# Performance work log

Hardware: AMD Instinct MI355X
Metric: run time of the kernel (lower is better)

## Reference

```python
import jax, jax.numpy as jnp
import numpy as np

N, X_DIM, Z_DIM, H = 4096, 256, 128, 512
NUM_ACTIONS = 4
TEMPERATURE = 0.1


def _init_linear(key, fan_in, fan_out):
    kw, kb = jax.random.split(key)
    bound = 1.0 / np.sqrt(fan_in)
    W = jax.random.uniform(kw, (fan_in, fan_out), minval=-bound, maxval=bound, dtype=jnp.float32)
    b = jax.random.uniform(kb, (fan_out,), minval=-bound, maxval=bound, dtype=jnp.float32)
    return W, b


def setup_inputs() -> dict:
    key = jax.random.key(0)
    ks = jax.random.split(key, 9)
    s = jax.random.normal(ks[0], (N, X_DIM), dtype=jnp.float32)
    sp = jax.random.normal(ks[1], (N, X_DIM), dtype=jnp.float32)
    a = jax.random.randint(ks[2], (N,), 0, NUM_ACTIONS)
    a1h = jax.nn.one_hot(a, NUM_ACTIONS, dtype=jnp.float32)
    # phi: x_dim -> 512 -> 512 -> z_dim
    pW0, pb0 = _init_linear(ks[3], X_DIM, H)
    pW1, pb1 = _init_linear(ks[4], H, H)
    pW2, pb2 = _init_linear(ks[5], H, Z_DIM)
    # g: x_dim + 4 -> 512 -> 512 -> z_dim
    gW0, gb0 = _init_linear(ks[6], X_DIM + NUM_ACTIONS, H)
    gW1, gb1 = _init_linear(ks[7], H, H)
    gW2, gb2 = _init_linear(ks[8], H, Z_DIM)
    return {"s": s, "sp": sp, "a1h": a1h,
            "pW0": pW0, "pb0": pb0, "pW1": pW1, "pb1": pb1, "pW2": pW2, "pb2": pb2,
            "gW0": gW0, "gb0": gb0, "gW1": gW1, "gb1": gb1, "gW2": gW2, "gb2": gb2}


def _mlp(x, W0, b0, W1, b1, W2, b2):
    h = jax.nn.relu(x @ W0 + b0)
    h = jax.nn.relu(h @ W1 + b1)
    return h @ W2 + b2


def reference(s, sp, a1h, pW0, pb0, pW1, pb1, pW2, pb2, gW0, gb0, gW1, gb1, gW2, gb2):
    z = _mlp(s, pW0, pb0, pW1, pb1, pW2, pb2)                      # [N, D]
    zpos = _mlp(jnp.concatenate([sp, a1h], axis=-1), gW0, gb0, gW1, gb1, gW2, gb2)  # [N, D]
    # -||z_i - zpos_j||^2 / T via the GEMM trick (avoids the [N,N,D] diff tensor)
    sq_z = jnp.sum(z * z, axis=-1, keepdims=True)                  # [N, 1]
    sq_p = jnp.sum(zpos * zpos, axis=-1)                            # [N]
    logits = -(sq_z + sq_p[None, :] - 2.0 * z @ zpos.T) / TEMPERATURE  # [N, N]
    # cross-entropy with targets = arange(N): diagonal is the positive
    log_probs = jax.nn.log_softmax(logits, axis=-1)
    loss = -jnp.mean(jnp.diagonal(log_probs))
    return loss
```

## Files before the change

kernel.cpp:

```cpp
#include <hip/hip_runtime.h>
#include <math.h>

#define NR 4096
#define ZD 128
#define HD 512
#define NJR 32
#define INV_T 10.0f

typedef __attribute__((ext_vector_type(8))) short bf16x8;
typedef __attribute__((ext_vector_type(4))) short short4v;
typedef __attribute__((ext_vector_type(4))) float f32x4;

typedef const unsigned int __attribute__((address_space(1)))* gas_t;
typedef unsigned int __attribute__((address_space(3)))* las_t;

__device__ __forceinline__ unsigned short f2bf(float f) {
  union { float f; unsigned u; } v; v.f = f;
  unsigned r = v.u + 0x7fff + ((v.u >> 16) & 1);
  return (unsigned short)(r >> 16);
}
__device__ __forceinline__ float bf2f(unsigned short b) {
  union { unsigned u; float f; } v; v.u = ((unsigned)b) << 16;
  return v.f;
}


__global__ __launch_bounds__(256) void prep(
    const float* __restrict__ s, const float* __restrict__ sp,
    const float* __restrict__ a1h,
    unsigned short* __restrict__ Sb, unsigned short* __restrict__ SPb,
    int* __restrict__ aidx,
    const float* __restrict__ pW0, unsigned short* __restrict__ pW0t,
    const float* __restrict__ pW1, unsigned short* __restrict__ pW1t,
    const float* __restrict__ pW2, unsigned short* __restrict__ pW2t,
    const float* __restrict__ gW0, unsigned short* __restrict__ gW0t,
    const float* __restrict__ gW1, unsigned short* __restrict__ gW1t,
    const float* __restrict__ gW2, unsigned short* __restrict__ gW2t,
    float* __restrict__ out) {
  int b = blockIdx.x, tid = threadIdx.x;
  if (b < 16) {
    int r = b * 256 + tid;
    int a = 0;
#pragma unroll
    for (int j = 0; j < 4; ++j) if (a1h[(size_t)r * 4 + j] > 0.5f) a = j;
    aidx[r] = a;
    if (b == 0 && tid == 0) out[0] = 0.f;
    return;
  }
  const int idx8 = tid & 127;
  const int h = idx8 & 1, p = idx8 >> 1, hi = p >> 4, l15 = p & 15;
  if (b < 2064) {
    const float* src = (b < 1040) ? s : sp;
    unsigned short* dst = (b < 1040) ? Sb : SPb;
    int lb = (b < 1040) ? b - 16 : b - 1040;
    int s0 = lb * 2 + (tid >> 7);
    int rf = s0 >> 3, ks = s0 & 7;
    int row = rf * 16 + l15, c0 = ks * 32 + hi * 4 + h * 16;
    float4 v = *(const float4*)&src[(size_t)row * 256 + c0];
    short4v o = { (short)f2bf(v.x), (short)f2bf(v.y), (short)f2bf(v.z), (short)f2bf(v.w) };
    *(short4v*)((char*)dst + (size_t)s0 * 1024 + idx8 * 8) = o;
    return;
  }
  int local = b - 2064;
  const float* W; unsigned short* Wt; int N, ksh;
  if (local < 128)      { W = pW0; Wt = pW0t; N = 512; ksh = 3; }
  else if (local < 384) { W = pW1; Wt = pW1t; N = 512; ksh = 4; local -= 128; }
  else if (local < 448) { W = pW2; Wt = pW2t; N = 128; ksh = 4; local -= 384; }
  else if (local < 576) { W = gW0; Wt = gW0t; N = 512; ksh = 3; local -= 448; }
  else if (local < 832) { W = gW1; Wt = gW1t; N = 512; ksh = 4; local -= 576; }
  else                  { W = gW2; Wt = gW2t; N = 128; ksh = 4; local -= 832; }
  int s0 = local * 2 + (tid >> 7);
  int rf = s0 >> ksh, ks = s0 & ((1 << ksh) - 1);
  int n = rf * 16 + l15, k0 = ks * 32 + hi * 4 + h * 16;
  short4v o = { (short)f2bf(W[(size_t)(k0 + 0) * N + n]),
                (short)f2bf(W[(size_t)(k0 + 1) * N + n]),
                (short)f2bf(W[(size_t)(k0 + 2) * N + n]),
                (short)f2bf(W[(size_t)(k0 + 3) * N + n]) };
  *(short4v*)((char*)Wt + (size_t)s0 * 1024 + idx8 * 8) = o;
}

template <bool RELU, bool GB, bool SQ, int K>
__global__ __launch_bounds__(256) void gemm_lds(
    const unsigned short* __restrict__ A0, const unsigned short* __restrict__ A1,
    const unsigned short* __restrict__ W0, const unsigned short* __restrict__ W1,
    const float* __restrict__ b0, const float* __restrict__ b1,
    unsigned short* __restrict__ C0, unsigned short* __restrict__ C1,
    float* __restrict__ sqp2, int N,
    const int* __restrict__ aidx, const float* __restrict__ gW0f) {
  __shared__ char As[2][16384];
  __shared__ char Bs[2][16384];
  constexpr int KS = K >> 5;
  constexpr int NSTEP = K >> 6;
  const int tid = threadIdx.x, lane = tid & 63, w = tid >> 6;
  const int wm = w >> 1, wn = w & 1;
  const int z = blockIdx.z;
  const char* Ab = (const char*)(z ? A1 : A0);
  const char* Wb = (const char*)(z ? W1 : W0);
  const float* bias = z ? b1 : b0;
  char* Cb = (char*)(z ? C1 : C0);
  const int bm = blockIdx.x * 128, bn = blockIdx.y * 128;
  const int lane16 = lane * 16;

  const char* asrc[4];
  const char* bsrc[4];
#pragma unroll
  for (int u = 0; u < 4; ++u) {
    const int sl = w * 4 + u;
    asrc[u] = Ab + (size_t)(((bm >> 4) + (sl >> 1)) * KS + (sl & 1)) * 1024 + lane16;
    bsrc[u] = Wb + (size_t)(((bn >> 4) + (sl >> 1)) * KS + (sl & 1)) * 1024 + lane16;
  }
  auto stage = [&](int buf, int st) {
    const int so = st * 2048;
#pragma unroll
    for (int u = 0; u < 4; ++u) {
      const int sl = w * 4 + u;
      __builtin_amdgcn_global_load_lds((gas_t)(asrc[u] + so), (las_t)&As[buf][sl * 1024], 16, 0, 0);
      __builtin_amdgcn_global_load_lds((gas_t)(bsrc[u] + so), (las_t)&Bs[buf][sl * 1024], 16, 0, 0);
    }
  };

  f32x4 acc[4][4] = {};
  stage(0, 0);
#pragma unroll
  for (int st = 0; st < NSTEP; ++st) {
    const int buf = st & 1;
    if (st + 1 < NSTEP) {
      stage(buf ^ 1, st + 1);
      asm volatile("s_waitcnt vmcnt(8)" ::: "memory");
    } else {
      asm volatile("s_waitcnt vmcnt(0)" ::: "memory");
    }
    __builtin_amdgcn_s_barrier();
    __builtin_amdgcn_sched_barrier(0);
#pragma unroll
    for (int kss = 0; kss < 2; ++kss) {
      bf16x8 af[4], bfv[4];
#pragma unroll
      for (int i = 0; i < 4; ++i)
        af[i] = *(const bf16x8*)(&As[buf][((wm * 4 + i) * 2 + kss) * 1024 + lane16]);
#pragma unroll
      for (int j = 0; j < 4; ++j)
        bfv[j] = *(const bf16x8*)(&Bs[buf][((wn * 4 + j) * 2 + kss) * 1024 + lane16]);
#pragma unroll
      for (int i = 0; i < 4; ++i)
#pragma unroll
        for (int j = 0; j < 4; ++j)
          acc[i][j] = __builtin_amdgcn_mfma_f32_16x16x32_bf16(bfv[j], af[i], acc[i][j], 0, 0, 0);
    }
    __builtin_amdgcn_sched_barrier(0);
    __builtin_amdgcn_s_barrier();
  }

  const int l15 = lane & 15, hi = lane >> 4;
  const int NS = N >> 5;
  const int row0 = bm + wm * 64;
  const int col0 = bn + wn * 64;
  float sq[4] = {0.f, 0.f, 0.f, 0.f};
  int ar[4] = {0, 0, 0, 0};
  if (GB && z == 1) {
#pragma unroll
    for (int i = 0; i < 4; ++i) ar[i] = aidx[row0 + i * 16 + l15];
  }
#pragma unroll
  for (int i = 0; i < 4; ++i) {
    const int rfC = (row0 >> 4) + i;
#pragma unroll
    for (int q = 0; q < 2; ++q) {
      float4 bi0 = *(const float4*)&bias[col0 + q * 32 + hi * 4];
      float4 bi1 = *(const float4*)&bias[col0 + q * 32 + 16 + hi * 4];
      float v[8] = { acc[i][2 * q][0] + bi0.x, acc[i][2 * q][1] + bi0.y,
                     acc[i][2 * q][2] + bi0.z, acc[i][2 * q][3] + bi0.w,
                     acc[i][2 * q + 1][0] + bi1.x, acc[i][2 * q + 1][1] + bi1.y,
                     acc[i][2 * q + 1][2] + bi1.z, acc[i][2 * q + 1][3] + bi1.w };
      if (GB && z == 1) {
        float4 g0 = *(const float4*)&gW0f[(size_t)(256 + ar[i]) * N + col0 + q * 32 + hi * 4];
        float4 g1 = *(const float4*)&gW0f[(size_t)(256 + ar[i]) * N + col0 + q * 32 + 16 + hi * 4];
        v[0] += g0.x; v[1] += g0.y; v[2] += g0.z; v[3] += g0.w;
        v[4] += g1.x; v[5] += g1.y; v[6] += g1.z; v[7] += g1.w;
      }
      bf16x8 r;
#pragma unroll
      for (int t = 0; t < 8; ++t) {
        float vv = RELU ? fmaxf(v[t], 0.f) : v[t];
        unsigned short cv = f2bf(vv);
        r[t] = (short)cv;
        if (SQ) { float vb = bf2f(cv); sq[i] += vb * vb; }
      }
      *(bf16x8*)(Cb + (size_t)(rfC * NS + ((col0 + q * 32) >> 5)) * 1024 + lane16) = r;
    }
  }
  if (SQ && z == 1) {
#pragma unroll
    for (int i = 0; i < 4; ++i) {
      float t = sq[i];
      t += __shfl_xor(t, 16, 64);
      t += __shfl_xor(t, 32, 64);
      if (lane < 16) sqp2[(size_t)wn * NR + row0 + i * 16 + lane] = t;
    }
  }
}

__global__ __launch_bounds__(256) void logits_fm(
    const unsigned short* __restrict__ Zb, const unsigned short* __restrict__ Zpb,
    const float* __restrict__ sqp2, float* __restrict__ wm_,
    float* __restrict__ wsum, float* __restrict__ wdiag) {
  __shared__ char Ps[32768];
  const int tid = threadIdx.x, lane = tid & 63, w = tid >> 6;
  const int l15 = lane & 15, hi = lane >> 4;
  const int i0 = blockIdx.x * 128, jr = blockIdx.y;
  const int row32 = i0 + w * 32;
  const int jbase = jr * 128;
  const int lane16 = lane * 16;
  const char* Zc = (const char*)Zb;
  const char* Pc = (const char*)Zpb;

  {
    const char* src = Pc + (size_t)jbase * 256;
#pragma unroll
    for (int u = 0; u < 8; ++u) {
      const int sl = w * 8 + u;
      __builtin_amdgcn_global_load_lds((gas_t)(src + sl * 1024 + lane16),
                                       (las_t)&Ps[sl * 1024], 16, 0, 0);
    }
  }
  bf16x8 afr[2][4];
#pragma unroll
  for (int rf = 0; rf < 2; ++rf)
#pragma unroll
    for (int ks = 0; ks < 4; ++ks)
      afr[rf][ks] = *(const bf16x8*)(Zc + (size_t)(((row32 >> 4) + rf) * 4 + ks) * 1024 + lane16);

  asm volatile("s_waitcnt vmcnt(0)" ::: "memory");
  __builtin_amdgcn_s_barrier();
  __builtin_amdgcn_sched_barrier(0);

  f32x4 acc[2][8] = {};
#pragma unroll
  for (int ks = 0; ks < 4; ++ks)
#pragma unroll
    for (int jf = 0; jf < 8; ++jf) {
      bf16x8 bfv = *(const bf16x8*)(&Ps[(jf * 4 + ks) * 1024 + lane16]);
      acc[0][jf] = __builtin_amdgcn_mfma_f32_16x16x32_bf16(bfv, afr[0][ks], acc[0][jf], 0, 0, 0);
      acc[1][jf] = __builtin_amdgcn_mfma_f32_16x16x32_bf16(bfv, afr[1][ks], acc[1][jf], 0, 0, 0);
    }

  f32x4 spq[8];
#pragma unroll
  for (int jf = 0; jf < 8; ++jf) {
    float4 s0 = *(const float4*)&sqp2[jbase + jf * 16 + hi * 4];
    float4 s1 = *(const float4*)&sqp2[NR + jbase + jf * 16 + hi * 4];
    spq[jf][0] = s0.x + s1.x; spq[jf][1] = s0.y + s1.y;
    spq[jf][2] = s0.z + s1.z; spq[jf][3] = s0.w + s1.w;
  }

#pragma unroll
  for (int rf = 0; rf < 2; ++rf) {
    const int grow = row32 + rf * 16 + l15;
    float mx = -INFINITY, dd = 0.f;
    bool hasd = false;
#pragma unroll
    for (int jf = 0; jf < 8; ++jf)
#pragma unroll
      for (int e = 0; e < 4; ++e) {
        const int j = jbase + jf * 16 + hi * 4 + e;
        float lv = (2.f * acc[rf][jf][e] - spq[jf][e]) * INV_T;
        acc[rf][jf][e] = lv;
        mx = fmaxf(mx, lv);
        if (j == grow) { dd = lv; hasd = true; }
      }
    mx = fmaxf(mx, __shfl_xor(mx, 16, 64));
    mx = fmaxf(mx, __shfl_xor(mx, 32, 64));
    float sum = 0.f;
#pragma unroll
    for (int jf = 0; jf < 8; ++jf)
#pragma unroll
      for (int e = 0; e < 4; ++e) sum += __expf(acc[rf][jf][e] - mx);
    sum += __shfl_xor(sum, 16, 64);
    sum += __shfl_xor(sum, 32, 64);
    if (hi == 0) {
      wm_[(size_t)jr * NR + grow] = mx;
      wsum[(size_t)jr * NR + grow] = sum;
    }
    if (hasd) wdiag[grow] = dd;
  }
}

__global__ __launch_bounds__(256) void finalize(const float* __restrict__ wm,
    const float* __restrict__ wsum, const float* __restrict__ wdiag,
    float* __restrict__ out) {
  int r = blockIdx.x * 256 + threadIdx.x;
  float mm = wm[r];
  float ss = wsum[r];
#pragma unroll
  for (int p = 1; p < NJR; ++p) {
    float mo = wm[(size_t)p * NR + r];
    float so = wsum[(size_t)p * NR + r];
    float mn = fmaxf(mm, mo);
    ss = ss * __expf(mm - mn) + so * __expf(mo - mn);
    mm = mn;
  }
  float loss_r = mm + logf(ss) - wdiag[r];
  float v = loss_r;
#pragma unroll
  for (int off = 32; off; off >>= 1) v += __shfl_xor(v, off, 64);
  __shared__ float partial[4];
  if ((threadIdx.x & 63) == 0) partial[threadIdx.x >> 6] = v;
  __syncthreads();
  if (threadIdx.x == 0)
    atomicAdd(out, (partial[0] + partial[1] + partial[2] + partial[3]) * (1.0f / (float)NR));
}

extern "C" void kernel_launch(void* const* d_in, const int* in_sizes, int n_in,
                              void* d_out, int out_size, void* d_ws, size_t ws_size,
                              hipStream_t stream) {
  const float* s   = (const float*)d_in[0];
  const float* sp  = (const float*)d_in[1];
  const float* a1h = (const float*)d_in[2];
  const float* pW0 = (const float*)d_in[3];
  const float* pb0 = (const float*)d_in[4];
  const float* pW1 = (const float*)d_in[5];
  const float* pb1 = (const float*)d_in[6];
  const float* pW2 = (const float*)d_in[7];
  const float* pb2 = (const float*)d_in[8];
  const float* gW0 = (const float*)d_in[9];
  const float* gb0 = (const float*)d_in[10];
  const float* gW1 = (const float*)d_in[11];
  const float* gb1 = (const float*)d_in[12];
  const float* gW2 = (const float*)d_in[13];
  const float* gb2 = (const float*)d_in[14];

  char* p = (char*)d_ws;
  unsigned short* Sb   = (unsigned short*)p; p += (size_t)NR * 256 * 2;
  unsigned short* SPb  = (unsigned short*)p; p += (size_t)NR * 256 * 2;
  unsigned short* H1   = (unsigned short*)p; p += (size_t)2 * NR * HD * 2;
  unsigned short* H2   = (unsigned short*)p; p += (size_t)2 * NR * HD * 2;
  unsigned short* Zall = (unsigned short*)p; p += (size_t)2 * NR * ZD * 2;
  unsigned short* pW0t = (unsigned short*)p; p += (size_t)256 * 512 * 2;
  unsigned short* pW1t = (unsigned short*)p; p += (size_t)512 * 512 * 2;
  unsigned short* pW2t = (unsigned short*)p; p += (size_t)512 * 128 * 2;
  unsigned short* gW0t = (unsigned short*)p; p += (size_t)256 * 512 * 2;
  unsigned short* gW1t = (unsigned short*)p; p += (size_t)512 * 512 * 2;
  unsigned short* gW2t = (unsigned short*)p; p += (size_t)512 * 128 * 2;
  float* sqp2 = (float*)p; p += (size_t)4 * NR * 4;
  float* wm   = (float*)p; p += (size_t)NJR * NR * 4;
  float* wsm  = (float*)p; p += (size_t)NJR * NR * 4;
  float* wdg  = (float*)p; p += (size_t)NR * 4;
  int*   aidx = (int*)p;  p += (size_t)NR * 4;

  unsigned short* H1g = H1 + (size_t)NR * HD;
  unsigned short* H2g = H2 + (size_t)NR * HD;
  unsigned short* Zb  = Zall;
  unsigned short* Zpb = Zall + (size_t)NR * ZD;

  dim3 blk(256);
  prep<<<2960, blk, 0, stream>>>(s, sp, a1h, Sb, SPb, aidx,
                                 pW0, pW0t, pW1, pW1t, pW2, pW2t,
                                 gW0, gW0t, gW1, gW1t, gW2, gW2t,
                                 (float*)d_out);

  gemm_lds<true, true, false, 256><<<dim3(32, 4, 2), blk, 0, stream>>>(
      Sb, SPb, pW0t, gW0t, pb0, gb0, H1, H1g, nullptr, 512, aidx, gW0);
  gemm_lds<true, false, false, 512><<<dim3(32, 4, 2), blk, 0, stream>>>(
      H1, H1g, pW1t, gW1t, pb1, gb1, H2, H2g, nullptr, 512, nullptr, nullptr);
  gemm_lds<false, false, true, 512><<<dim3(32, 1, 2), blk, 0, stream>>>(
      H2, H2g, pW2t, gW2t, pb2, gb2, Zb, Zpb, sqp2, 128, nullptr, nullptr);

  logits_fm<<<dim3(NR / 128, NJR), blk, 0, stream>>>(Zb, Zpb, sqp2, wm, wsm, wdg);
  finalize<<<NR / 256, blk, 0, stream>>>(wm, wsm, wdg, (float*)d_out);
}
```

Measured before the change: 56.40 us.

## Use smaller GEMM tiles with triple-buffered LDS pipeline and drop LDS in logits

The MLP GEMM kernel moves to a narrower 64-column tile, with a BM template parameter so the last layer can use 64-row tiles. This multiplies the block count to fill more CUs. Its LDS staging goes from double to triple buffering, with prefetch two steps ahead and matching vmcnt waits. The logits kernel no longer stages Zpos through LDS and reads B fragments directly from global memory. The squared-norm partials are now split four ways, so logits sums four slices. Smaller tiles lower per-block reuse and raise global traffic, and direct global B reads in logits may add latency.

```diff
diff --git a/kernel.cpp b/kernel.cpp
--- a/kernel.cpp
+++ b/kernel.cpp
@@ -79,18 +79,25 @@
   *(short4v*)((char*)Wt + (size_t)s0 * 1024 + idx8 * 8) = o;
 }
 
-template <bool RELU, bool GB, bool SQ, int K>
-__global__ __launch_bounds__(256) void gemm_lds(
+template <int BM, int K, bool RELU, bool GB, bool SQ>
+__global__ __launch_bounds__(256) void gemm_p3(
     const unsigned short* __restrict__ A0, const unsigned short* __restrict__ A1,
     const unsigned short* __restrict__ W0, const unsigned short* __restrict__ W1,
     const float* __restrict__ b0, const float* __restrict__ b1,
     unsigned short* __restrict__ C0, unsigned short* __restrict__ C1,
     float* __restrict__ sqp2, int N,
     const int* __restrict__ aidx, const float* __restrict__ gW0f) {
-  __shared__ char As[2][16384];
-  __shared__ char Bs[2][16384];
   constexpr int KS = K >> 5;
   constexpr int NSTEP = K >> 6;
+  constexpr int ABYTES = BM * 128;
+  constexpr int BBYTES = 8192;
+  constexpr int NA = BM >> 5;
+  constexpr int WM_FR = BM >> 5;
+  constexpr int V = NA + 2;
+  __shared__ char lds[3 * (ABYTES + BBYTES)];
+  char* AsB = lds;
+  char* BsB = lds + 3 * ABYTES;
+
   const int tid = threadIdx.x, lane = tid & 63, w = tid >> 6;
   const int wm = w >> 1, wn = w & 1;
   const int z = blockIdx.z;
@@ -98,104 +105,103 @@
   const char* Wb = (const char*)(z ? W1 : W0);
   const float* bias = z ? b1 : b0;
   char* Cb = (char*)(z ? C1 : C0);
-  const int bm = blockIdx.x * 128, bn = blockIdx.y * 128;
+  const int bm = blockIdx.x * BM, bn = blockIdx.y * 64;
   const int lane16 = lane * 16;
 
-  const char* asrc[4];
-  const char* bsrc[4];
-#pragma unroll
-  for (int u = 0; u < 4; ++u) {
-    const int sl = w * 4 + u;
-    asrc[u] = Ab + (size_t)(((bm >> 4) + (sl >> 1)) * KS + (sl & 1)) * 1024 + lane16;
-    bsrc[u] = Wb + (size_t)(((bn >> 4) + (sl >> 1)) * KS + (sl & 1)) * 1024 + lane16;
-  }
   auto stage = [&](int buf, int st) {
-    const int so = st * 2048;
-#pragma unroll
-    for (int u = 0; u < 4; ++u) {
-      const int sl = w * 4 + u;
-      __builtin_amdgcn_global_load_lds((gas_t)(asrc[u] + so), (las_t)&As[buf][sl * 1024], 16, 0, 0);
-      __builtin_amdgcn_global_load_lds((gas_t)(bsrc[u] + so), (las_t)&Bs[buf][sl * 1024], 16, 0, 0);
+#pragma unroll
+    for (int u = 0; u < NA; ++u) {
+      const int sl = w * NA + u;
+      const char* src = Ab + ((size_t)((bm >> 4) + (sl >> 1)) * KS + st * 2 + (sl & 1)) * 1024 + lane16;
+      __builtin_amdgcn_global_load_lds((gas_t)src, (las_t)(AsB + buf * ABYTES + sl * 1024), 16, 0, 0);
+    }
+#pragma unroll
+    for (int u = 0; u < 2; ++u) {
+      const int sl = w * 2 + u;
+      const char* src = Wb + ((size_t)((bn >> 4) + (sl >> 1)) * KS + st * 2 + (sl & 1)) * 1024 + lane16;
+      __builtin_amdgcn_global_load_lds((gas_t)src, (las_t)(BsB + buf * BBYTES + sl * 1024), 16, 0, 0);
     }
   };
 
-  f32x4 acc[4][4] = {};
+  f32x4 acc[WM_FR][2] = {};
   stage(0, 0);
+  stage(1, 1);
 #pragma unroll
   for (int st = 0; st < NSTEP; ++st) {
-    const int buf = st & 1;
-    if (st + 1 < NSTEP) {
-      stage(buf ^ 1, st + 1);
-      asm volatile("s_waitcnt vmcnt(8)" ::: "memory");
+    const int buf = st % 3;
+    if (st + 2 < NSTEP) {
+      stage((st + 2) % 3, st + 2);
+      if constexpr (V == 6) asm volatile("s_waitcnt vmcnt(12)" ::: "memory");
+      else                  asm volatile("s_waitcnt vmcnt(8)" ::: "memory");
+    } else if (st + 1 < NSTEP) {
+      if constexpr (V == 6) asm volatile("s_waitcnt vmcnt(6)" ::: "memory");
+      else                  asm volatile("s_waitcnt vmcnt(4)" ::: "memory");
     } else {
       asm volatile("s_waitcnt vmcnt(0)" ::: "memory");
     }
     __builtin_amdgcn_s_barrier();
-    __builtin_amdgcn_sched_barrier(0);
 #pragma unroll
     for (int kss = 0; kss < 2; ++kss) {
-      bf16x8 af[4], bfv[4];
-#pragma unroll
-      for (int i = 0; i < 4; ++i)
-        af[i] = *(const bf16x8*)(&As[buf][((wm * 4 + i) * 2 + kss) * 1024 + lane16]);
-#pragma unroll
-      for (int j = 0; j < 4; ++j)
-        bfv[j] = *(const bf16x8*)(&Bs[buf][((wn * 4 + j) * 2 + kss) * 1024 + lane16]);
-#pragma unroll
-      for (int i = 0; i < 4; ++i)
-#pragma unroll
-        for (int j = 0; j < 4; ++j)
+      bf16x8 af[WM_FR], bfv[2];
+#pragma unroll
+      for (int i = 0; i < WM_FR; ++i)
+        af[i] = *(const bf16x8*)(AsB + buf * ABYTES + ((wm * WM_FR + i) * 2 + kss) * 1024 + lane16);
+#pragma unroll
+      for (int j = 0; j < 2; ++j)
+        bfv[j] = *(const bf16x8*)(BsB + buf * BBYTES + ((wn * 2 + j) * 2 + kss) * 1024 + lane16);
+#pragma unroll
+      for (int i = 0; i < WM_FR; ++i)
+#pragma unroll
+        for (int j = 0; j < 2; ++j)
           acc[i][j] = __builtin_amdgcn_mfma_f32_16x16x32_bf16(bfv[j], af[i], acc[i][j], 0, 0, 0);
     }
-    __builtin_amdgcn_sched_barrier(0);
     __builtin_amdgcn_s_barrier();
   }
 
   const int l15 = lane & 15, hi = lane >> 4;
   const int NS = N >> 5;
-  const int row0 = bm + wm * 64;
-  const int col0 = bn + wn * 64;
-  float sq[4] = {0.f, 0.f, 0.f, 0.f};
-  int ar[4] = {0, 0, 0, 0};
+  const int row0 = bm + wm * (BM / 2);
+  const int col0 = bn + wn * 32;
+  float sq[WM_FR];
+  int ar[WM_FR];
+#pragma unroll
+  for (int i = 0; i < WM_FR; ++i) { sq[i] = 0.f; ar[i] = 0; }
   if (GB && z == 1) {
 #pragma unroll
-    for (int i = 0; i < 4; ++i) ar[i] = aidx[row0 + i * 16 + l15];
-  }
-#pragma unroll
-  for (int i = 0; i < 4; ++i) {
+    for (int i = 0; i < WM_FR; ++i) ar[i] = aidx[row0 + i * 16 + l15];
+  }
+  float4 bi0 = *(const float4*)&bias[col0 + hi * 4];
+  float4 bi1 = *(const float4*)&bias[col0 + 16 + hi * 4];
+#pragma unroll
+  for (int i = 0; i < WM_FR; ++i) {
     const int rfC = (row0 >> 4) + i;
-#pragma unroll
-    for (int q = 0; q < 2; ++q) {
-      float4 bi0 = *(const float4*)&bias[col0 + q * 32 + hi * 4];
-      float4 bi1 = *(const float4*)&bias[col0 + q * 32 + 16 + hi * 4];
-      float v[8] = { acc[i][2 * q][0] + bi0.x, acc[i][2 * q][1] + bi0.y,
-                     acc[i][2 * q][2] + bi0.z, acc[i][2 * q][3] + bi0.w,
-                     acc[i][2 * q + 1][0] + bi1.x, acc[i][2 * q + 1][1] + bi1.y,
-                     acc[i][2 * q + 1][2] + bi1.z, acc[i][2 * q + 1][3] + bi1.w };
-      if (GB && z == 1) {
-        float4 g0 = *(const float4*)&gW0f[(size_t)(256 + ar[i]) * N + col0 + q * 32 + hi * 4];
-        float4 g1 = *(const float4*)&gW0f[(size_t)(256 + ar[i]) * N + col0 + q * 32 + 16 + hi * 4];
-        v[0] += g0.x; v[1] += g0.y; v[2] += g0.z; v[3] += g0.w;
-        v[4] += g1.x; v[5] += g1.y; v[6] += g1.z; v[7] += g1.w;
-      }
-      bf16x8 r;
-#pragma unroll
-      for (int t = 0; t < 8; ++t) {
-        float vv = RELU ? fmaxf(v[t], 0.f) : v[t];
-        unsigned short cv = f2bf(vv);
-        r[t] = (short)cv;
-        if (SQ) { float vb = bf2f(cv); sq[i] += vb * vb; }
-      }
-      *(bf16x8*)(Cb + (size_t)(rfC * NS + ((col0 + q * 32) >> 5)) * 1024 + lane16) = r;
-    }
+    float v[8] = { acc[i][0][0] + bi0.x, acc[i][0][1] + bi0.y,
+                   acc[i][0][2] + bi0.z, acc[i][0][3] + bi0.w,
+                   acc[i][1][0] + bi1.x, acc[i][1][1] + bi1.y,
+                   acc[i][1][2] + bi1.z, acc[i][1][3] + bi1.w };
+    if (GB && z == 1) {
+      float4 g0 = *(const float4*)&gW0f[(size_t)(256 + ar[i]) * N + col0 + hi * 4];
+      float4 g1 = *(const float4*)&gW0f[(size_t)(256 + ar[i]) * N + col0 + 16 + hi * 4];
+      v[0] += g0.x; v[1] += g0.y; v[2] += g0.z; v[3] += g0.w;
+      v[4] += g1.x; v[5] += g1.y; v[6] += g1.z; v[7] += g1.w;
+    }
+    bf16x8 r;
+#pragma unroll
+    for (int t = 0; t < 8; ++t) {
+      float vv = RELU ? fmaxf(v[t], 0.f) : v[t];
+      unsigned short cv = f2bf(vv);
+      r[t] = (short)cv;
+      if (SQ) { float vb = bf2f(cv); sq[i] += vb * vb; }
+    }
+    *(bf16x8*)(Cb + (size_t)(rfC * NS + (col0 >> 5)) * 1024 + lane16) = r;
   }
   if (SQ && z == 1) {
 #pragma unroll
-    for (int i = 0; i < 4; ++i) {
+    for (int i = 0; i < WM_FR; ++i) {
       float t = sq[i];
       t += __shfl_xor(t, 16, 64);
       t += __shfl_xor(t, 32, 64);
-      if (lane < 16) sqp2[(size_t)wn * NR + row0 + i * 16 + lane] = t;
+      if (lane < 16) sqp2[(size_t)(col0 >> 5) * NR + row0 + i * 16 + lane] = t;
     }
   }
 }
@@ -204,7 +210,6 @@
     const unsigned short* __restrict__ Zb, const unsigned short* __restrict__ Zpb,
     const float* __restrict__ sqp2, float* __restrict__ wm_,
     float* __restrict__ wsum, float* __restrict__ wdiag) {
-  __shared__ char Ps[32768];
   const int tid = threadIdx.x, lane = tid & 63, w = tid >> 6;
   const int l15 = lane & 15, hi = lane >> 4;
   const int i0 = blockIdx.x * 128, jr = blockIdx.y;
@@ -214,15 +219,6 @@
   const char* Zc = (const char*)Zb;
   const char* Pc = (const char*)Zpb;
 
-  {
-    const char* src = Pc + (size_t)jbase * 256;
-#pragma unroll
-    for (int u = 0; u < 8; ++u) {
-      const int sl = w * 8 + u;
-      __builtin_amdgcn_global_load_lds((gas_t)(src + sl * 1024 + lane16),
-                                       (las_t)&Ps[sl * 1024], 16, 0, 0);
-    }
-  }
   bf16x8 afr[2][4];
 #pragma unroll
   for (int rf = 0; rf < 2; ++rf)
@@ -230,27 +226,16 @@
     for (int ks = 0; ks < 4; ++ks)
       afr[rf][ks] = *(const bf16x8*)(Zc + (size_t)(((row32 >> 4) + rf) * 4 + ks) * 1024 + lane16);
 
-  asm volatile("s_waitcnt vmcnt(0)" ::: "memory");
-  __builtin_amdgcn_s_barrier();
-  __builtin_amdgcn_sched_barrier(0);
-
   f32x4 acc[2][8] = {};
 #pragma unroll
-  for (int ks = 0; ks < 4; ++ks)
-#pragma unroll
-    for (int jf = 0; jf < 8; ++jf) {
-      bf16x8 bfv = *(const bf16x8*)(&Ps[(jf * 4 + ks) * 1024 + lane16]);
+  for (int jf = 0; jf < 8; ++jf) {
+    const size_t js = (size_t)((jbase >> 4) + jf) * 4;
+#pragma unroll
+    for (int ks = 0; ks < 4; ++ks) {
+      bf16x8 bfv = *(const bf16x8*)(Pc + (js + ks) * 1024 + lane16);
       acc[0][jf] = __builtin_amdgcn_mfma_f32_16x16x32_bf16(bfv, afr[0][ks], acc[0][jf], 0, 0, 0);
       acc[1][jf] = __builtin_amdgcn_mfma_f32_16x16x32_bf16(bfv, afr[1][ks], acc[1][jf], 0, 0, 0);
     }
-
-  f32x4 spq[8];
-#pragma unroll
-  for (int jf = 0; jf < 8; ++jf) {
-    float4 s0 = *(const float4*)&sqp2[jbase + jf * 16 + hi * 4];
-    float4 s1 = *(const float4*)&sqp2[NR + jbase + jf * 16 + hi * 4];
-    spq[jf][0] = s0.x + s1.x; spq[jf][1] = s0.y + s1.y;
-    spq[jf][2] = s0.z + s1.z; spq[jf][3] = s0.w + s1.w;
   }
 
 #pragma unroll
@@ -259,15 +244,22 @@
     float mx = -INFINITY, dd = 0.f;
     bool hasd = false;
 #pragma unroll
-    for (int jf = 0; jf < 8; ++jf)
+    for (int jf = 0; jf < 8; ++jf) {
+      const int cb = jbase + jf * 16 + hi * 4;
+      float4 q0 = *(const float4*)&sqp2[cb];
+      float4 q1 = *(const float4*)&sqp2[NR + cb];
+      float4 q2 = *(const float4*)&sqp2[2 * NR + cb];
+      float4 q3 = *(const float4*)&sqp2[3 * NR + cb];
+      float sp[4] = { q0.x + q1.x + q2.x + q3.x, q0.y + q1.y + q2.y + q3.y,
+                      q0.z + q1.z + q2.z + q3.z, q0.w + q1.w + q2.w + q3.w };
 #pragma unroll
       for (int e = 0; e < 4; ++e) {
-        const int j = jbase + jf * 16 + hi * 4 + e;
-        float lv = (2.f * acc[rf][jf][e] - spq[jf][e]) * INV_T;
+        float lv = (2.f * acc[rf][jf][e] - sp[e]) * INV_T;
         acc[rf][jf][e] = lv;
         mx = fmaxf(mx, lv);
-        if (j == grow) { dd = lv; hasd = true; }
+        if (cb + e == grow) { dd = lv; hasd = true; }
       }
+    }
     mx = fmaxf(mx, __shfl_xor(mx, 16, 64));
     mx = fmaxf(mx, __shfl_xor(mx, 32, 64));
     float sum = 0.f;
@@ -358,11 +350,11 @@
                                  gW0, gW0t, gW1, gW1t, gW2, gW2t,
                                  (float*)d_out);
 
-  gemm_lds<true, true, false, 256><<<dim3(32, 4, 2), blk, 0, stream>>>(
+  gemm_p3<128, 256, true, true, false><<<dim3(32, 8, 2), blk, 0, stream>>>(
       Sb, SPb, pW0t, gW0t, pb0, gb0, H1, H1g, nullptr, 512, aidx, gW0);
-  gemm_lds<true, false, false, 512><<<dim3(32, 4, 2), blk, 0, stream>>>(
+  gemm_p3<128, 512, true, false, false><<<dim3(32, 8, 2), blk, 0, stream>>>(
       H1, H1g, pW1t, gW1t, pb1, gb1, H2, H2g, nullptr, 512, nullptr, nullptr);
-  gemm_lds<false, false, true, 512><<<dim3(32, 1, 2), blk, 0, stream>>>(
+  gemm_p3<64, 512, false, false, true><<<dim3(64, 2, 2), blk, 0, stream>>>(
       H2, H2g, pW2t, gW2t, pb2, gb2, Zb, Zpb, sqp2, 128, nullptr, nullptr);
 
   logits_fm<<<dim3(NR / 128, NJR), blk, 0, stream>>>(Zb, Zpb, sqp2, wm, wsm, wdg);
```

Measured after the change: 54.47 us. 1.04x faster.
